# Kernel tuning notes

Measured on AMD Instinct MI355X. Metric: run time of the kernel, lower is better.

The kernel has to match this reference:

```python
import jax, jax.numpy as jnp
import numpy as np

ROTARY_BASE = 10000
INFTY_APPROX = 1e30
B, T, M, H, D = 2, 2048, 2048, 16, 128


def rope(x):
    # x: [B, T, H, D]; half-split rotary encoding
    *_, length, _, width = x.shape
    half = width // 2
    positions = jnp.arange(length, dtype=jnp.float32)[None, :, None, None]      # [1,T,1,1]
    dims = jnp.arange(half, dtype=jnp.float32)
    ang_freqs = jnp.power(float(ROTARY_BASE), -dims / half)[None, None, None, :]  # [1,1,1,D/2]
    radians = positions * ang_freqs
    cos = jnp.cos(radians).astype(x.dtype)
    sin = jnp.sin(radians).astype(x.dtype)
    even, odd = x[..., :half], x[..., half:]
    r_even = even * cos - odd * sin
    r_odd = even * sin + odd * cos
    return jnp.concatenate([r_even, r_odd], axis=-1)


def setup_inputs() -> dict:
    key = jax.random.key(0)
    k0, k1, k2, k3, k4 = jax.random.split(key, 5)
    return {
        "x": jax.random.normal(k0, (B, T, M), dtype=jnp.float32),
        "w_aq": jax.random.normal(k1, (H, M, D), dtype=jnp.float32) * (M ** -0.5),
        "w_ak": jax.random.normal(k2, (H, M, D), dtype=jnp.float32) * (M ** -0.5),
        "w_av": jax.random.normal(k3, (H, M, D), dtype=jnp.float32) * (M ** -0.5),
        "w_ao": jax.random.normal(k4, (H, D, M), dtype=jnp.float32) * ((2 * 24 * M) ** -0.5),
    }


def reference(x, w_aq, w_ak, w_av, w_ao):
    q = jnp.einsum("btm,hmd->bthd", x, w_aq)
    k = jnp.einsum("btm,hmd->bthd", x, w_ak)
    v = jnp.einsum("btm,hmd->bthd", x, w_av)
    q = rope(q)
    k = rope(k)
    # muP attention scaling: 1/d_head (not 1/sqrt(d_head))
    mult = (1.0 / D) ** 0.5
    s = jnp.einsum("bihd,bjhd->bhij", mult * q, mult * k)  # [B,H,T,T]
    i = jnp.arange(T)[:, None]
    j = jnp.arange(T)[None, :]
    mask = (i < j)[None, None, :, :]  # mask future positions
    s = s - jnp.asarray(INFTY_APPROX, dtype=x.dtype) * mask
    p = jax.nn.softmax(s, axis=-1)
    o = jnp.einsum("bhij,bjhd->bihd", p, v)
    r = jnp.einsum("bihd,hdm->bim", o, w_ao)
    return r
```

## Files before the change

### kernel.cpp

```cpp
#include <hip/hip_runtime.h>

#define Bb 2
#define Tt 2048
#define Mm 2048
#define Hh 16
#define Dd 128

typedef __attribute__((ext_vector_type(8))) short bf16x8;
typedef __attribute__((ext_vector_type(4))) float f32x4;
typedef __attribute__((ext_vector_type(16))) float f32x16;

__device__ __forceinline__ unsigned short f2bf(float f) {
    unsigned int u = __builtin_bit_cast(unsigned int, f);
    u += 0x7FFFu + ((u >> 16) & 1u);
    return (unsigned short)(u >> 16);
}

__device__ __forceinline__ unsigned int cvt_pk_bf16(float lo, float hi) {
    unsigned int r;
    asm("v_cvt_pk_bf16_f32 %0, %1, %2" : "=v"(r) : "v"(lo), "v"(hi));
    return r;
}

__device__ __forceinline__ float fexp2(float x) { return __builtin_amdgcn_exp2f(x); }

__device__ __forceinline__ void gld16(const void* g, void* l) {
    __builtin_amdgcn_global_load_lds(
        (const __attribute__((address_space(1))) void*)g,
        (__attribute__((address_space(3))) void*)l, 16, 0, 0);
}


__global__ __launch_bounds__(256) void cvt_x2(const float* __restrict__ x,
                                              unsigned short* __restrict__ xb2) {
    const int blk = blockIdx.x;
    const int mt = blk >> 5, kt = blk & 31;
#pragma unroll
    for (int it = 0; it < 4; ++it) {
        int s = it * 256 + threadIdx.x;
        int row = ((s >> 6) & 3) * 32 + (s & 31);
        int k = (s >> 8) * 16 + ((s >> 5) & 1) * 8;
        const float* sp = x + ((long)(mt * 128 + row)) * 2048 + kt * 64 + k;
        float4 a = *(const float4*)sp;
        float4 b = *(const float4*)(sp + 4);
        uint4 pk;
        pk.x = (unsigned int)f2bf(a.x) | ((unsigned int)f2bf(a.y) << 16);
        pk.y = (unsigned int)f2bf(a.z) | ((unsigned int)f2bf(a.w) << 16);
        pk.z = (unsigned int)f2bf(b.x) | ((unsigned int)f2bf(b.y) << 16);
        pk.w = (unsigned int)f2bf(b.z) | ((unsigned int)f2bf(b.w) << 16);
        *(uint4*)(xb2 + (((long)(mt * 32 + kt)) * 1024 + s) * 8) = pk;
    }
}

__global__ __launch_bounds__(256) void w_qkv_tile(
    const float* __restrict__ wq, const float* __restrict__ wk, const float* __restrict__ wv,
    unsigned short* __restrict__ outBase) {
    __shared__ float tile[64][132];
    const int kt = blockIdx.x;
    const int zy = blockIdx.y;
    const int which = zy >> 4, head = zy & 15;
    const float* src = (which == 0 ? wq : which == 1 ? wk : wv) + (long)head * 2048 * 128;
    const int tid = threadIdx.x;
#pragma unroll
    for (int it = 0; it < 8; ++it) {
        int f = it * 256 + tid;
        int row = f >> 5, c4 = f & 31;
        float4 v = *(const float4*)(src + (long)(kt * 64 + row) * 128 + c4 * 4);
        tile[row][c4 * 4 + 0] = v.x;
        tile[row][c4 * 4 + 1] = v.y;
        tile[row][c4 * 4 + 2] = v.z;
        tile[row][c4 * 4 + 3] = v.w;
    }
    __syncthreads();
    unsigned short* outp = outBase + (((long)(which * 16 + head)) * 32 + kt) * 1024 * 8;
#pragma unroll
    for (int it = 0; it < 4; ++it) {
        int up = it * 256 + tid;
        int kk = up >> 8, nf = (up >> 6) & 3, l = up & 63;
        int il = l & 31, hl = l >> 5;
        int d = il + 64 * (nf & 1) + 32 * (nf >> 1);
        int kl = kk * 16 + hl * 8;
        uint4 pk;
        pk.x = (unsigned int)f2bf(tile[kl + 0][d]) | ((unsigned int)f2bf(tile[kl + 1][d]) << 16);
        pk.y = (unsigned int)f2bf(tile[kl + 2][d]) | ((unsigned int)f2bf(tile[kl + 3][d]) << 16);
        pk.z = (unsigned int)f2bf(tile[kl + 4][d]) | ((unsigned int)f2bf(tile[kl + 5][d]) << 16);
        pk.w = (unsigned int)f2bf(tile[kl + 6][d]) | ((unsigned int)f2bf(tile[kl + 7][d]) << 16);
        *(uint4*)(outp + (long)up * 8) = pk;
    }
}

__global__ __launch_bounds__(256) void transpose_cvt(const float* __restrict__ in,
                                                     unsigned short* __restrict__ out,
                                                     int rows, int cols,
                                                     long in_slab, long out_slab) {
    __shared__ float tile[32][33];
    const float* ip = in + (long)blockIdx.z * in_slab;
    unsigned short* op = out + (long)blockIdx.z * out_slab;
    int r0 = blockIdx.x * 32, c0 = blockIdx.y * 32;
    int tx = threadIdx.x & 31, ty = threadIdx.x >> 5;
#pragma unroll
    for (int j = 0; j < 32; j += 8)
        tile[ty + j][tx] = ip[(long)(r0 + ty + j) * cols + c0 + tx];
    __syncthreads();
#pragma unroll
    for (int j = 0; j < 32; j += 8)
        op[(long)(c0 + ty + j) * rows + r0 + tx] = f2bf(tile[tx][ty + j]);
}

__global__ __launch_bounds__(256) void rope_tab(float* __restrict__ cosT,
                                                float* __restrict__ sinT) {
    int idx = blockIdx.x * 256 + threadIdx.x;
    int t = idx >> 6, d = idx & 63;
    float freq = powf(10000.f, -(float)d / 64.f);
    float ang = (float)t * freq;
    sinT[idx] = sinf(ang);
    cosT[idx] = cosf(ang);
}

template <bool WIDE>
__device__ __forceinline__ void proj_sub10(
    const unsigned short* __restrict__ xb2,
    const unsigned short* __restrict__ wT2,
    char* lds, int bm, int offc,
    unsigned short* __restrict__ qO, unsigned short* __restrict__ kO,
    unsigned short* __restrict__ vtO,
    const float* __restrict__ cosT, const float* __restrict__ sinT, int tid) {
    const int lane = tid & 63, wave = tid >> 6;
    const int il = lane & 31, hl = lane >> 5;
    const int wm = WIDE ? (wave >> 2) : (wave >> 1);
    const int wn = WIDE ? (wave & 3) : (wave & 1);
    const int hseg0 = offc >> 7;
    const int mode = offc >> 11;
    constexpr int MF = WIDE ? 4 : 2;

    f32x16 acc[MF][2];
#pragma unroll
    for (int a = 0; a < MF; ++a)
#pragma unroll
        for (int b2 = 0; b2 < 2; ++b2)
#pragma unroll
            for (int e = 0; e < 16; ++e) acc[a][b2][e] = 0.f;

    auto stageTo = [&](int buf, int kt) {
        char* dst = lds + buf * 65536;
#pragma unroll
        for (int i = 0; i < 4; ++i) {
            int f = i * 512 + tid;
            int sub = f >> 10, s = f & 1023;
            gld16(xb2 + (((long)((2 * bm + sub) * 32 + kt)) * 1024 + s) * 8, dst + f * 16);
        }
        if (WIDE) {
#pragma unroll
            for (int i = 0; i < 4; ++i) {
                int g = i * 512 + tid;
                int hs = g >> 10, u = g & 1023;
                gld16(wT2 + (((long)((hseg0 + hs) * 32 + kt)) * 1024 + u) * 8,
                      dst + 32768 + g * 16);
            }
        } else {
#pragma unroll
            for (int i = 0; i < 2; ++i) {
                int g = i * 512 + tid;
                gld16(wT2 + (((long)(hseg0 * 32 + kt)) * 1024 + g) * 8,
                      dst + 32768 + g * 16);
            }
        }
    };

    stageTo(0, 0);

    for (int t = 0; t < 32; ++t) {
        const int cur = t & 1;
        if (t + 1 < 32) {
            stageTo(cur ^ 1, t + 1);
            if (WIDE) asm volatile("s_waitcnt vmcnt(8)" ::: "memory");
            else      asm volatile("s_waitcnt vmcnt(6)" ::: "memory");
        } else {
            asm volatile("s_waitcnt vmcnt(0)" ::: "memory");
        }
        __builtin_amdgcn_s_barrier();

        const char* bc = lds + cur * 65536;
        __builtin_amdgcn_s_setprio(1);
#pragma unroll
        for (int kk = 0; kk < 4; ++kk) {
            bf16x8 af[MF], bf[2];
#pragma unroll
            for (int mf = 0; mf < MF; ++mf) {
                int chunk = WIDE ? (wm * 1024 + kk * 256 + mf * 64 + lane)
                                 : ((wm >> 1) * 1024 + kk * 256 + ((wm & 1) * 2 + mf) * 64 + lane);
                af[mf] = *(const bf16x8*)(bc + chunk * 16);
            }
#pragma unroll
            for (int nf2 = 0; nf2 < 2; ++nf2) {
                int chunk = WIDE ? ((wn >> 1) * 1024 + kk * 256 + ((wn & 1) * 2 + nf2) * 64 + lane)
                                 : (kk * 256 + (wn * 2 + nf2) * 64 + lane);
                bf[nf2] = *(const bf16x8*)(bc + 32768 + chunk * 16);
            }
#pragma unroll
            for (int mf = 0; mf < MF; ++mf)
#pragma unroll
                for (int nf2 = 0; nf2 < 2; ++nf2)
                    acc[mf][nf2] = __builtin_amdgcn_mfma_f32_32x32x16_bf16(
                        af[mf], bf[nf2], acc[mf][nf2], 0, 0, 0);
        }
        __builtin_amdgcn_s_setprio(0);
        asm volatile("" ::: "memory");
        __builtin_amdgcn_s_barrier();
    }

    const int b = bm >> 3;
    const int t0 = (bm & 7) * 256;
    const int head_g = WIDE ? (hseg0 + (wn >> 1)) : hseg0;
    const int head_l = head_g & 15;
    const int opar = WIDE ? (wn & 1) : wn;
    constexpr int WMS = WIDE ? 128 : 64;

    if (mode < 2) {
        const float qs = (mode == 0) ? 0.011271055f : 1.0f;
        unsigned short* outp = (mode == 0) ? qO : kO;
        long hb = ((long)(b * Hh + head_l)) * Tt;
        int d_lo = il + 32 * opar;
#pragma unroll
        for (int mf = 0; mf < MF; ++mf)
#pragma unroll
            for (int reg = 0; reg < 16; ++reg) {
                int r = (reg & 3) + 8 * (reg >> 2) + 4 * hl;
                int tt = t0 + wm * WMS + mf * 32 + r;
                float c = cosT[tt * 64 + d_lo], s = sinT[tt * 64 + d_lo];
                float ev = acc[mf][0][reg], od = acc[mf][1][reg];
                long base = (hb + tt) * Dd;
                outp[base + d_lo]      = f2bf((ev * c - od * s) * qs);
                outp[base + d_lo + 64] = f2bf((ev * s + od * c) * qs);
            }
    } else {
        __syncthreads();
        char* patch = lds + wave * 4096;
        long hdbase = ((long)(b * Hh + head_l)) * Dd * Tt;
#pragma unroll
        for (int mf = 0; mf < MF; ++mf) {
#pragma unroll
            for (int nf = 0; nf < 2; ++nf) {
                int dslot = nf * 32 + il;
                int swz = (dslot & 3) << 4;
#pragma unroll
                for (int qg = 0; qg < 4; ++qg) {
                    uint2 w;
                    w.x = cvt_pk_bf16(acc[mf][nf][qg * 4 + 0], acc[mf][nf][qg * 4 + 1]);
                    w.y = cvt_pk_bf16(acc[mf][nf][qg * 4 + 2], acc[mf][nf][qg * 4 + 3]);
                    *(uint2*)(patch + dslot * 64 + ((qg * 16 + hl * 8) ^ swz)) = w;
                }
            }
            __builtin_amdgcn_s_waitcnt(0);
#pragma unroll
            for (int p2 = 0; p2 < 4; ++p2) {
                int dslot = p2 * 16 + (lane >> 2);
                int t8 = lane & 3;
                uint4 v = *(const uint4*)(patch + dslot * 64 + ((t8 * 16) ^ ((dslot & 3) << 4)));
                int o = opar * 2 + (dslot >> 5), il2 = dslot & 31;
                int dd = il2 + 32 * (o >> 1) + 64 * (o & 1);
                int tg = t0 + wm * WMS + mf * 32 + t8 * 8;
                *(uint4*)(vtO + hdbase + (long)dd * Tt + tg) = v;
            }
            __builtin_amdgcn_s_waitcnt(0);
        }
    }
}

__global__ __launch_bounds__(512, 2) void proj_gemm10(
    const unsigned short* __restrict__ xb2,
    const unsigned short* __restrict__ wT2,
    unsigned short* __restrict__ qO,
    unsigned short* __restrict__ kO,
    unsigned short* __restrict__ vtO,
    const float* __restrict__ cosT,
    const float* __restrict__ sinT) {
    __shared__ __align__(16) char lds[131072];
    const int bm = blockIdx.x;
    const int bc = blockIdx.y;
    const int s = bc * 384;
    const bool swap = ((s & 2047) == 1920);
    const int offw = swap ? s + 128 : s;
    const int offn = swap ? s : s + 256;
    const int tid = threadIdx.x;

    proj_sub10<true>(xb2, wT2, lds, bm, offw, qO, kO, vtO, cosT, sinT, tid);
    __syncthreads();
    proj_sub10<false>(xb2, wT2, lds, bm, offn, qO, kO, vtO, cosT, sinT, tid);
}

__global__ __launch_bounds__(256) void attn_kernel(
    const unsigned short* __restrict__ q,
    const unsigned short* __restrict__ k,
    const unsigned short* __restrict__ vt,
    unsigned short* __restrict__ o) {
    __shared__ __align__(16) unsigned short lds[32768];

    const int lid = (int)blockIdx.x;
    const int p = lid & 255;
    const int bh = p & 31;
    const int q0 = p >> 5;
    const int qb = (lid >> 8) ? (15 - q0) : q0;

    const int tid = threadIdx.x, lane = tid & 63, wave = tid >> 6;
    const int h = lane >> 5, iln = lane & 31;

    const unsigned short* qp = q + (long)bh * Tt * Dd;
    const unsigned short* kp = k + (long)bh * Tt * Dd;
    const unsigned short* vp = vt + (long)bh * Dd * Tt;

    const int i_g = qb * 128 + wave * 32 + iln;
    bf16x8 qf[8];
#pragma unroll
    for (int kk = 0; kk < 8; ++kk)
        qf[kk] = *(const bf16x8*)(qp + (long)i_g * Dd + kk * 16 + h * 8);

    f32x16 accO[4];
#pragma unroll
    for (int nb = 0; nb < 4; ++nb)
#pragma unroll
        for (int e = 0; e < 16; ++e) accO[nb][e] = 0.f;

    float m_r = -1e30f, l_r = 0.f;
    const int ntiles = 2 * qb + 2;

    auto stage = [&](int buf, int tix) {
        const int j0s = tix * 64;
#pragma unroll
        for (int it = 0; it < 4; ++it) {
            int f = it * 256 + tid;
            int rk = f >> 4, ck = f & 15;
            gld16(kp + ((long)(j0s + rk) * Dd + ((ck ^ (rk & 7)) << 3)),
                  (char*)lds + buf * 16384 + f * 16);
            int rv = f >> 3, cv = f & 7;
            gld16(vp + ((long)rv * Tt + j0s + ((cv ^ (rv & 7)) << 3)),
                  (char*)lds + 32768 + buf * 16384 + f * 16);
        }
    };

    stage(0, 0);

    for (int tix = 0; tix < ntiles; ++tix) {
        const int cur = tix & 1;
        const int j0 = tix * 64;
        if (tix + 1 < ntiles) {
            stage(cur ^ 1, tix + 1);
            asm volatile("s_waitcnt vmcnt(8)" ::: "memory");
        } else {
            asm volatile("s_waitcnt vmcnt(0)" ::: "memory");
        }
        __builtin_amdgcn_s_barrier();

        const char* Kb = (const char*)lds + cur * 16384;
        const char* Vb = (const char*)lds + 32768 + cur * 16384;

        f32x16 sacc[2];
#pragma unroll
        for (int mb = 0; mb < 2; ++mb)
#pragma unroll
            for (int e = 0; e < 16; ++e) sacc[mb][e] = 0.f;

        __builtin_amdgcn_s_setprio(1);
#pragma unroll
        for (int mb = 0; mb < 2; ++mb) {
            int row = mb * 32 + iln;
            const char* Kr = Kb + row * 256;
            int sw = row & 7;
#pragma unroll
            for (int kk = 0; kk < 8; ++kk) {
                bf16x8 kf = *(const bf16x8*)(Kr + 16 * ((kk * 2 + h) ^ sw));
                sacc[mb] = __builtin_amdgcn_mfma_f32_32x32x16_bf16(kf, qf[kk], sacc[mb], 0, 0, 0);
            }
        }
        __builtin_amdgcn_s_setprio(0);

        const bool domask = (j0 + 63 > qb * 128);
        if (domask) {
#pragma unroll
            for (int mb = 0; mb < 2; ++mb)
#pragma unroll
                for (int reg = 0; reg < 16; ++reg) {
                    int j = j0 + mb * 32 + (reg & 3) + 8 * (reg >> 2) + 4 * h;
                    if (j > i_g) sacc[mb][reg] = -1e30f;
                }
        }

        float red[16];
#pragma unroll
        for (int r = 0; r < 16; ++r) red[r] = fmaxf(sacc[0][r], sacc[1][r]);
#pragma unroll
        for (int s = 8; s >= 1; s >>= 1)
#pragma unroll
            for (int r = 0; r < s; ++r) red[r] = fmaxf(red[r], red[r + s]);
        float mx = fmaxf(red[0], __shfl_xor(red[0], 32, 64));

        if (__any(mx > m_r + 8.f)) {
            float mn = fmaxf(m_r, mx);
            float corr = fexp2(m_r - mn);
            m_r = mn;
            l_r *= corr;
#pragma unroll
            for (int reg = 0; reg < 16; ++reg) {
                int rrow = (reg & 3) + 8 * (reg >> 2) + 4 * h;
                float c = __shfl(corr, rrow, 64);
#pragma unroll
                for (int nb = 0; nb < 4; ++nb) accO[nb][reg] *= c;
            }
        }

        float pe[2][16];
#pragma unroll
        for (int mb = 0; mb < 2; ++mb)
#pragma unroll
            for (int r = 0; r < 16; ++r) pe[mb][r] = fexp2(sacc[mb][r] - m_r);
        float sr[16];
#pragma unroll
        for (int r = 0; r < 16; ++r) sr[r] = pe[0][r] + pe[1][r];
#pragma unroll
        for (int s = 8; s >= 1; s >>= 1)
#pragma unroll
            for (int r = 0; r < s; ++r) sr[r] += sr[r + s];
        l_r += sr[0] + __shfl_xor(sr[0], 32, 64);

        unsigned int pu[2][8];
#pragma unroll
        for (int mb = 0; mb < 2; ++mb)
#pragma unroll
            for (int t = 0; t < 8; ++t)
                pu[mb][t] = cvt_pk_bf16(pe[mb][2 * t], pe[mb][2 * t + 1]);

        unsigned int rv2[2][4];
#pragma unroll
        for (int mb = 0; mb < 2; ++mb)
#pragma unroll
            for (int u = 0; u < 4; ++u) {
                unsigned int sv = h ? pu[mb][(u & 1) + 4 * (u >> 1)]
                                    : pu[mb][2 + (u & 1) + 4 * (u >> 1)];
                rv2[mb][u] = __shfl_xor(sv, 32, 64);
            }

        __builtin_amdgcn_s_setprio(1);
#pragma unroll
        for (int kk2 = 0; kk2 < 4; ++kk2) {
            const int mb = kk2 >> 1, c2 = kk2 & 1;
            unsigned int w0 = h ? rv2[mb][2 * c2 + 0] : pu[mb][4 * c2 + 0];
            unsigned int w1 = h ? rv2[mb][2 * c2 + 1] : pu[mb][4 * c2 + 1];
            unsigned int w2 = h ? pu[mb][4 * c2 + 2] : rv2[mb][2 * c2 + 0];
            unsigned int w3 = h ? pu[mb][4 * c2 + 3] : rv2[mb][2 * c2 + 1];
            uint4 aw; aw.x = w0; aw.y = w1; aw.z = w2; aw.w = w3;
            bf16x8 af = __builtin_bit_cast(bf16x8, aw);
#pragma unroll
            for (int nb = 0; nb < 4; ++nb) {
                int dd = nb * 32 + iln;
                int byte = dd * 128 + 16 * ((kk2 * 2 + h) ^ (dd & 7));
                bf16x8 vf = *(const bf16x8*)(Vb + byte);
                accO[nb] = __builtin_amdgcn_mfma_f32_32x32x16_bf16(af, vf, accO[nb], 0, 0, 0);
            }
        }
        __builtin_amdgcn_s_setprio(0);

        asm volatile("" ::: "memory");
        __builtin_amdgcn_s_barrier();
    }

    const int b = bh >> 4, hh = bh & 15;
    float invl = 1.f / l_r;
#pragma unroll
    for (int reg = 0; reg < 16; ++reg) {
        int rrow = (reg & 3) + 8 * (reg >> 2) + 4 * h;
        float iv = __shfl(invl, rrow, 64);
        int t = qb * 128 + wave * 32 + rrow;
        long base = ((long)(b * Tt + t) * Hh + hh) * Dd;
#pragma unroll
        for (int nb = 0; nb < 4; ++nb)
            o[base + nb * 32 + iln] = f2bf(accO[nb][reg] * iv);
    }
}

__global__ __launch_bounds__(256) void out_gemm(
    const unsigned short* __restrict__ oIn,
    const unsigned short* __restrict__ woT,
    float* __restrict__ out) {
    __shared__ __align__(16) unsigned short smem[32768];
    const int bm = blockIdx.x, bn = blockIdx.y;
    const int tid = threadIdx.x;
    const int lane = tid & 63;
    const int wave = tid >> 6;
    const int g = lane >> 4;
    const int ln = lane & 15;

    const unsigned short* arow = oIn + (long)bm * 128 * Mm;
    const unsigned short* brow = woT + (long)bn * 128 * Mm;

    f32x4 acc[2][8];
#pragma unroll
    for (int a = 0; a < 2; ++a)
#pragma unroll
        for (int b2 = 0; b2 < 8; ++b2)
#pragma unroll
            for (int e = 0; e < 4; ++e) acc[a][b2][e] = 0.f;

    auto stage = [&](int buf, int kt) {
        const int k0 = kt * 64;
#pragma unroll
        for (int it = 0; it < 4; ++it) {
            int f = it * 256 + tid;
            int r = f >> 3, c = f & 7;
            long off = (long)r * Mm + k0 + ((c ^ (r & 7)) << 3);
            gld16(arow + off, (char*)smem + buf * 32768 + f * 16);
            gld16(brow + off, (char*)smem + buf * 32768 + 16384 + f * 16);
        }
    };

    stage(0, 0);

    for (int kt = 0; kt < Mm / 64; ++kt) {
        const int cur = kt & 1;
        asm volatile("s_waitcnt vmcnt(0)" ::: "memory");
        __builtin_amdgcn_s_barrier();
        if (kt + 1 < Mm / 64) stage(cur ^ 1, kt + 1);

        const char* Ab = (const char*)smem + cur * 32768;
        const char* Bv = Ab + 16384;
#pragma unroll
        for (int kc = 0; kc < 2; ++kc) {
            bf16x8 af[2];
#pragma unroll
            for (int rf = 0; rf < 2; ++rf) {
                int row = wave * 32 + rf * 16 + ln;
                int byte = (row * 128 + kc * 64 + g * 16) ^ ((row & 7) << 4);
                af[rf] = *(const bf16x8*)(Ab + byte);
            }
#pragma unroll
            for (int ni = 0; ni < 8; ++ni) {
                int row = ni * 16 + ln;
                int byte = (row * 128 + kc * 64 + g * 16) ^ ((row & 7) << 4);
                bf16x8 bfv = *(const bf16x8*)(Bv + byte);
#pragma unroll
                for (int rf = 0; rf < 2; ++rf)
                    acc[rf][ni] = __builtin_amdgcn_mfma_f32_16x16x32_bf16(af[rf], bfv, acc[rf][ni], 0, 0, 0);
            }
        }
        asm volatile("" ::: "memory");
    }

#pragma unroll
    for (int rf = 0; rf < 2; ++rf)
#pragma unroll
        for (int reg = 0; reg < 4; ++reg) {
            long row = bm * 128 + wave * 32 + rf * 16 + g * 4 + reg;
#pragma unroll
            for (int ni = 0; ni < 8; ++ni)
                out[row * Mm + bn * 128 + ni * 16 + ln] = acc[rf][ni][reg];
        }
}


extern "C" void kernel_launch(void* const* d_in, const int* in_sizes, int n_in,
                              void* d_out, int out_size, void* d_ws, size_t ws_size,
                              hipStream_t stream) {
    const float* x    = (const float*)d_in[0];
    const float* w_aq = (const float*)d_in[1];
    const float* w_ak = (const float*)d_in[2];
    const float* w_av = (const float*)d_in[3];
    const float* w_ao = (const float*)d_in[4];
    float* out = (float*)d_out;

    char* ws = (char*)d_ws;
    const long SZ_BTM = 16777216;
    const long SZ_W   = 8388608;
    unsigned short* xb2 = (unsigned short*)(ws);
    unsigned short* qB  = (unsigned short*)(ws + SZ_BTM);
    unsigned short* kB  = (unsigned short*)(ws + 2 * SZ_BTM);
    unsigned short* vtB = (unsigned short*)(ws + 3 * SZ_BTM);
    unsigned short* oB  = (unsigned short*)(ws + 4 * SZ_BTM);
    unsigned short* wT2 = (unsigned short*)(ws + 5 * SZ_BTM);
    unsigned short* woT = (unsigned short*)(ws + 5 * SZ_BTM + 3 * SZ_W);
    float* cosT = (float*)(ws + 5 * SZ_BTM + 4 * SZ_W);
    float* sinT = (float*)(ws + 5 * SZ_BTM + 4 * SZ_W + 524288);

    cvt_x2<<<1024, 256, 0, stream>>>(x, xb2);
    w_qkv_tile<<<dim3(32, 48), 256, 0, stream>>>(w_aq, w_ak, w_av, wT2);
    transpose_cvt<<<dim3(64, 64, 1), 256, 0, stream>>>(w_ao, woT, 2048, 2048, 0, 0);
    rope_tab<<<512, 256, 0, stream>>>(cosT, sinT);

    proj_gemm10<<<dim3(16, 16), 512, 0, stream>>>(xb2, wT2, qB, kB, vtB, cosT, sinT);
    attn_kernel<<<dim3(512), 256, 0, stream>>>(qB, kB, vtB, oB);
    out_gemm<<<dim3(32, 16), 256, 0, stream>>>(oB, woT, out);
}
```

Before: 242.1 us.

## Pre-tile attention output and W_o into MFMA fragment layout for output GEMM

The attention kernel now stages its normalized output through LDS and writes it in a pre-swizzled MFMA-fragment tile layout, and W_o is converted into a matching tiled bf16 layout instead of a plain transpose. The output GEMM is rewritten as a 512-thread, 128x256-tile kernel using 32x32x16 MFMAs with contiguous 16-byte loads, prefetching the next stage before waiting, and priority hints. This is meant to remove LDS swizzle address math and bank conflicts and to raise arithmetic intensity per tile. In exchange it adds an extra LDS round-trip in the attention epilogue and uses larger LDS per block.

Measured after the change: 239.0 us. Within noise of the previous version (-1.3%).

```diff
diff --git a/kernel.cpp b/kernel.cpp
--- a/kernel.cpp
+++ b/kernel.cpp
@@ -89,22 +89,38 @@
     }
 }
 
-__global__ __launch_bounds__(256) void transpose_cvt(const float* __restrict__ in,
-                                                     unsigned short* __restrict__ out,
-                                                     int rows, int cols,
-                                                     long in_slab, long out_slab) {
-    __shared__ float tile[32][33];
-    const float* ip = in + (long)blockIdx.z * in_slab;
-    unsigned short* op = out + (long)blockIdx.z * out_slab;
-    int r0 = blockIdx.x * 32, c0 = blockIdx.y * 32;
-    int tx = threadIdx.x & 31, ty = threadIdx.x >> 5;
-#pragma unroll
-    for (int j = 0; j < 32; j += 8)
-        tile[ty + j][tx] = ip[(long)(r0 + ty + j) * cols + c0 + tx];
+__global__ __launch_bounds__(256) void w_o_tile(const float* __restrict__ wo,
+                                                unsigned short* __restrict__ wo2) {
+    __shared__ float tile[64][132];
+    const int kt = blockIdx.x;
+    const int nt = blockIdx.y;
+    const int tid = threadIdx.x;
+#pragma unroll
+    for (int it = 0; it < 8; ++it) {
+        int f = it * 256 + tid;
+        int row = f >> 5, c4 = f & 31;
+        float4 v = *(const float4*)(wo + (long)(kt * 64 + row) * 2048 + nt * 128 + c4 * 4);
+        tile[row][c4 * 4 + 0] = v.x;
+        tile[row][c4 * 4 + 1] = v.y;
+        tile[row][c4 * 4 + 2] = v.z;
+        tile[row][c4 * 4 + 3] = v.w;
+    }
     __syncthreads();
-#pragma unroll
-    for (int j = 0; j < 32; j += 8)
-        op[(long)(c0 + ty + j) * rows + r0 + tx] = f2bf(tile[tx][ty + j]);
+    unsigned short* outp = wo2 + (((long)(nt * 32 + kt)) * 1024) * 8;
+#pragma unroll
+    for (int it = 0; it < 4; ++it) {
+        int up = it * 256 + tid;
+        int kk = up >> 8, nf = (up >> 6) & 3, l = up & 63;
+        int il = l & 31, hl = l >> 5;
+        int n = nf * 32 + il;
+        int kl = kk * 16 + hl * 8;
+        uint4 pk;
+        pk.x = (unsigned int)f2bf(tile[kl + 0][n]) | ((unsigned int)f2bf(tile[kl + 1][n]) << 16);
+        pk.y = (unsigned int)f2bf(tile[kl + 2][n]) | ((unsigned int)f2bf(tile[kl + 3][n]) << 16);
+        pk.z = (unsigned int)f2bf(tile[kl + 4][n]) | ((unsigned int)f2bf(tile[kl + 5][n]) << 16);
+        pk.w = (unsigned int)f2bf(tile[kl + 6][n]) | ((unsigned int)f2bf(tile[kl + 7][n]) << 16);
+        *(uint4*)(outp + (long)up * 8) = pk;
+    }
 }
 
 __global__ __launch_bounds__(256) void rope_tab(float* __restrict__ cosT,
@@ -293,7 +309,7 @@
     const unsigned short* __restrict__ q,
     const unsigned short* __restrict__ k,
     const unsigned short* __restrict__ vt,
-    unsigned short* __restrict__ o) {
+    unsigned short* __restrict__ o2) {
     __shared__ __align__(16) unsigned short lds[32768];
 
     const int lid = (int)blockIdx.x;
@@ -465,94 +481,111 @@
 
     const int b = bh >> 4, hh = bh & 15;
     float invl = 1.f / l_r;
-#pragma unroll
-    for (int reg = 0; reg < 16; ++reg) {
-        int rrow = (reg & 3) + 8 * (reg >> 2) + 4 * h;
-        float iv = __shfl(invl, rrow, 64);
-        int t = qb * 128 + wave * 32 + rrow;
-        long base = ((long)(b * Tt + t) * Hh + hh) * Dd;
-#pragma unroll
-        for (int nb = 0; nb < 4; ++nb)
-            o[base + nb * 32 + iln] = f2bf(accO[nb][reg] * iv);
-    }
-}
-
-__global__ __launch_bounds__(256) void out_gemm(
-    const unsigned short* __restrict__ oIn,
-    const unsigned short* __restrict__ woT,
+    char* patch = (char*)lds + wave * 8192;
+#pragma unroll
+    for (int nb = 0; nb < 4; ++nb)
+#pragma unroll
+        for (int reg = 0; reg < 16; ++reg) {
+            int rrow = (reg & 3) + 8 * (reg >> 2) + 4 * h;
+            float iv = __shfl(invl, rrow, 64);
+            int d = nb * 32 + iln;
+            int byte = (d >> 6) * 4096 + ((d >> 4) & 3) * 1024 +
+                       (rrow + 32 * ((d >> 3) & 1)) * 16 + (d & 7) * 2;
+            *(unsigned short*)(patch + byte) = f2bf(accO[nb][reg] * iv);
+        }
+    asm volatile("s_waitcnt lgkmcnt(0)" ::: "memory");
+    const int mt = b * 16 + qb;
+#pragma unroll
+    for (int i = 0; i < 8; ++i) {
+        int c = i * 64 + lane;
+        int dh = c >> 8, kk4 = (c >> 6) & 3, slot = c & 63;
+        uint4 v = *(const uint4*)(patch + c * 16);
+        *(uint4*)(o2 + (((long)(mt * 32 + hh * 2 + dh)) * 1024 + kk4 * 256 + wave * 64 + slot) * 8) = v;
+    }
+}
+
+__global__ __launch_bounds__(512, 2) void out_gemm2(
+    const unsigned short* __restrict__ oB2,
+    const unsigned short* __restrict__ wo2,
     float* __restrict__ out) {
-    __shared__ __align__(16) unsigned short smem[32768];
-    const int bm = blockIdx.x, bn = blockIdx.y;
-    const int tid = threadIdx.x;
-    const int lane = tid & 63;
-    const int wave = tid >> 6;
-    const int g = lane >> 4;
-    const int ln = lane & 15;
-
-    const unsigned short* arow = oIn + (long)bm * 128 * Mm;
-    const unsigned short* brow = woT + (long)bn * 128 * Mm;
-
-    f32x4 acc[2][8];
+    __shared__ __align__(16) char lds[98304];
+    const int bm = blockIdx.x;
+    const int bn = blockIdx.y;
+    const int tid = threadIdx.x, lane = tid & 63, wave = tid >> 6;
+    const int il = lane & 31, hl = lane >> 5;
+    const int wm = wave >> 2, wn = wave & 3;
+
+    f32x16 acc[2][2];
 #pragma unroll
     for (int a = 0; a < 2; ++a)
 #pragma unroll
-        for (int b2 = 0; b2 < 8; ++b2)
-#pragma unroll
-            for (int e = 0; e < 4; ++e) acc[a][b2][e] = 0.f;
-
-    auto stage = [&](int buf, int kt) {
-        const int k0 = kt * 64;
-#pragma unroll
-        for (int it = 0; it < 4; ++it) {
-            int f = it * 256 + tid;
-            int r = f >> 3, c = f & 7;
-            long off = (long)r * Mm + k0 + ((c ^ (r & 7)) << 3);
-            gld16(arow + off, (char*)smem + buf * 32768 + f * 16);
-            gld16(brow + off, (char*)smem + buf * 32768 + 16384 + f * 16);
+        for (int b2 = 0; b2 < 2; ++b2)
+#pragma unroll
+            for (int e = 0; e < 16; ++e) acc[a][b2][e] = 0.f;
+
+    auto stageTo = [&](int buf, int kt) {
+        char* dst = lds + buf * 49152;
+#pragma unroll
+        for (int i = 0; i < 2; ++i) {
+            int f = i * 512 + tid;
+            gld16(oB2 + (((long)(bm * 32 + kt)) * 1024 + f) * 8, dst + f * 16);
+        }
+#pragma unroll
+        for (int i = 0; i < 4; ++i) {
+            int g = i * 512 + tid;
+            int sub = g >> 10, u = g & 1023;
+            gld16(wo2 + (((long)((bn * 2 + sub) * 32 + kt)) * 1024 + u) * 8,
+                  dst + 16384 + g * 16);
         }
     };
 
-    stage(0, 0);
-
-    for (int kt = 0; kt < Mm / 64; ++kt) {
-        const int cur = kt & 1;
-        asm volatile("s_waitcnt vmcnt(0)" ::: "memory");
+    stageTo(0, 0);
+
+    for (int t = 0; t < 32; ++t) {
+        const int cur = t & 1;
+        if (t + 1 < 32) {
+            stageTo(cur ^ 1, t + 1);
+            asm volatile("s_waitcnt vmcnt(6)" ::: "memory");
+        } else {
+            asm volatile("s_waitcnt vmcnt(0)" ::: "memory");
+        }
         __builtin_amdgcn_s_barrier();
-        if (kt + 1 < Mm / 64) stage(cur ^ 1, kt + 1);
-
-        const char* Ab = (const char*)smem + cur * 32768;
-        const char* Bv = Ab + 16384;
-#pragma unroll
-        for (int kc = 0; kc < 2; ++kc) {
-            bf16x8 af[2];
-#pragma unroll
-            for (int rf = 0; rf < 2; ++rf) {
-                int row = wave * 32 + rf * 16 + ln;
-                int byte = (row * 128 + kc * 64 + g * 16) ^ ((row & 7) << 4);
-                af[rf] = *(const bf16x8*)(Ab + byte);
-            }
-#pragma unroll
-            for (int ni = 0; ni < 8; ++ni) {
-                int row = ni * 16 + ln;
-                int byte = (row * 128 + kc * 64 + g * 16) ^ ((row & 7) << 4);
-                bf16x8 bfv = *(const bf16x8*)(Bv + byte);
-#pragma unroll
-                for (int rf = 0; rf < 2; ++rf)
-                    acc[rf][ni] = __builtin_amdgcn_mfma_f32_16x16x32_bf16(af[rf], bfv, acc[rf][ni], 0, 0, 0);
-            }
-        }
+
+        const char* bc = lds + cur * 49152;
+        __builtin_amdgcn_s_setprio(1);
+#pragma unroll
+        for (int kk = 0; kk < 4; ++kk) {
+            bf16x8 af[2], bf[2];
+#pragma unroll
+            for (int mf = 0; mf < 2; ++mf)
+                af[mf] = *(const bf16x8*)(bc + (kk * 256 + (wm * 2 + mf) * 64 + lane) * 16);
+#pragma unroll
+            for (int nf = 0; nf < 2; ++nf)
+                bf[nf] = *(const bf16x8*)(bc + 16384 + (wn >> 1) * 16384 +
+                                          (kk * 256 + ((wn & 1) * 2 + nf) * 64 + lane) * 16);
+#pragma unroll
+            for (int mf = 0; mf < 2; ++mf)
+#pragma unroll
+                for (int nf = 0; nf < 2; ++nf)
+                    acc[mf][nf] = __builtin_amdgcn_mfma_f32_32x32x16_bf16(
+                        af[mf], bf[nf], acc[mf][nf], 0, 0, 0);
+        }
+        __builtin_amdgcn_s_setprio(0);
         asm volatile("" ::: "memory");
-    }
-
-#pragma unroll
-    for (int rf = 0; rf < 2; ++rf)
-#pragma unroll
-        for (int reg = 0; reg < 4; ++reg) {
-            long row = bm * 128 + wave * 32 + rf * 16 + g * 4 + reg;
-#pragma unroll
-            for (int ni = 0; ni < 8; ++ni)
-                out[row * Mm + bn * 128 + ni * 16 + ln] = acc[rf][ni][reg];
-        }
+        __builtin_amdgcn_s_barrier();
+    }
+
+#pragma unroll
+    for (int mf = 0; mf < 2; ++mf)
+#pragma unroll
+        for (int nf = 0; nf < 2; ++nf)
+#pragma unroll
+            for (int reg = 0; reg < 16; ++reg) {
+                int r = (reg & 3) + 8 * (reg >> 2) + 4 * hl;
+                long row = bm * 128 + wm * 64 + mf * 32 + r;
+                int col = bn * 256 + (wn >> 1) * 128 + ((wn & 1) * 2 + nf) * 32 + il;
+                out[row * Mm + col] = acc[mf][nf][reg];
+            }
 }
 
 
@@ -573,18 +606,18 @@
     unsigned short* qB  = (unsigned short*)(ws + SZ_BTM);
     unsigned short* kB  = (unsigned short*)(ws + 2 * SZ_BTM);
     unsigned short* vtB = (unsigned short*)(ws + 3 * SZ_BTM);
-    unsigned short* oB  = (unsigned short*)(ws + 4 * SZ_BTM);
+    unsigned short* oB2 = (unsigned short*)(ws + 4 * SZ_BTM);
     unsigned short* wT2 = (unsigned short*)(ws + 5 * SZ_BTM);
-    unsigned short* woT = (unsigned short*)(ws + 5 * SZ_BTM + 3 * SZ_W);
+    unsigned short* wo2 = (unsigned short*)(ws + 5 * SZ_BTM + 3 * SZ_W);
     float* cosT = (float*)(ws + 5 * SZ_BTM + 4 * SZ_W);
     float* sinT = (float*)(ws + 5 * SZ_BTM + 4 * SZ_W + 524288);
 
     cvt_x2<<<1024, 256, 0, stream>>>(x, xb2);
     w_qkv_tile<<<dim3(32, 48), 256, 0, stream>>>(w_aq, w_ak, w_av, wT2);
-    transpose_cvt<<<dim3(64, 64, 1), 256, 0, stream>>>(w_ao, woT, 2048, 2048, 0, 0);
+    w_o_tile<<<dim3(32, 16), 256, 0, stream>>>(w_ao, wo2);
     rope_tab<<<512, 256, 0, stream>>>(cosT, sinT);
 
     proj_gemm10<<<dim3(16, 16), 512, 0, stream>>>(xb2, wT2, qB, kB, vtB, cosT, sinT);
-    attn_kernel<<<dim3(512), 256, 0, stream>>>(qB, kB, vtB, oB);
-    out_gemm<<<dim3(32, 16), 256, 0, stream>>>(oB, woT, out);
-}
+    attn_kernel<<<dim3(512), 256, 0, stream>>>(qB, kB, vtB, oB2);
+    out_gemm2<<<dim3(32, 8), 512, 0, stream>>>(oB2, wo2, out);
+}
```
